# Optimization experiments

Measured on AMD Instinct MI355X. Metric: run time of the kernel, lower is better.

Reference implementation:

```python
import jax, jax.numpy as jnp
import numpy as np

N, F_IN = 4096, 128
UNITS0, HEADS0 = 16, 4   # hidden GraphAttention layer
UNITS1, HEADS1 = 1, 1    # final layer (sigmoid, mean over last axis)


def _glorot(key, shape):
    fan_in, fan_out = shape[0], shape[1]
    std = (2.0 / (fan_in + fan_out)) ** 0.5
    return std * jax.random.normal(key, shape, dtype=jnp.float32)


def setup_inputs() -> dict:
    key = jax.random.key(0)
    ks = jax.random.split(key, 8)
    x = jax.random.normal(ks[0], (N, F_IN), dtype=jnp.float32)
    adj = (jax.random.uniform(ks[1], (N, N)) < 0.01).astype(jnp.float32)
    return {
        "x": x,
        "adj": adj,
        "w0": _glorot(ks[2], (F_IN, UNITS0)),
        "aw1_0": _glorot(ks[3], (UNITS0, HEADS0)),
        "aw2_0": _glorot(ks[4], (UNITS0, HEADS0)),
        "w1": _glorot(ks[5], (UNITS0 * HEADS0, UNITS1)),
        "aw1_1": _glorot(ks[6], (UNITS1, HEADS1)),
        "aw2_1": _glorot(ks[7], (UNITS1, HEADS1)),
    }


def _gat_layer(x, adj, w, aw1, aw2, activation, final_layer):
    h = x @ w                                   # [N, units]
    a1 = h @ aw1                                # [N, H]
    a2 = h @ aw2                                # [N, H]
    # relu(a1_i + a2_j) broadcast -> [N, N, H]
    coeffs = jax.nn.relu(a1[:, None, :] + a2[None, :, :])
    # elementwise adjacency mask then softmax over neighbor axis (axis=1),
    # matching tf.nn.softmax(adj * coeffs[:,:,i], axis=1)
    attn = jax.nn.softmax(adj[:, :, None] * coeffs, axis=1)   # [N, N, H]
    # per-head aggregation then concat heads: [N, H*units]
    out = jnp.einsum('ijh,jd->ihd', attn, h).reshape(h.shape[0], -1)
    if final_layer:
        out = out.mean(axis=-1)                 # [N]
    return activation(out)


def reference(x, adj, w0, aw1_0, aw2_0, w1, aw1_1, aw2_1):
    h = _gat_layer(x, adj, w0, aw1_0, aw2_0, jax.nn.relu, False)   # [N, 64]
    out = _gat_layer(h, adj, w1, aw1_1, aw2_1, jax.nn.sigmoid, True)  # [N]
    return out
```

## Files before the change

### kernel.cpp

```cpp
#include <hip/hip_runtime.h>
#include <hip/hip_bf16.h>

#define N 4096
#define FIN 128
#define U0 16
#define H0 4
#define MAXD 128
#define NGEMM (N / 16)
#define NCSR (N / 2)
#define FSTRIDE 32

__global__ void k1_fused(const float* __restrict__ adj, const float* __restrict__ x,
                         const float* __restrict__ w0, const float* __restrict__ aw1,
                         const float* __restrict__ aw2,
                         int* __restrict__ deg, int* __restrict__ cols,
                         float* __restrict__ F, float* __restrict__ a1,
                         float* __restrict__ partS0) {
    const int t = threadIdx.x;
    if (blockIdx.x < NGEMM) {
        const int bid = blockIdx.x;
        __shared__ float xs[16][FIN + 1];
        __shared__ float ws[FIN][U0];
        __shared__ float hs[16][U0 + 1];
        const int r0 = bid * 16;

        for (int k = t; k < FIN * U0; k += 256) ws[k / U0][k % U0] = w0[k];
        for (int k = t; k < 16 * FIN; k += 256)
            xs[k / FIN][k % FIN] = x[(size_t)(r0 + k / FIN) * FIN + (k % FIN)];
        __syncthreads();

        const int r = t / U0, u = t % U0;
        float acc = 0.f;
        #pragma unroll 8
        for (int k = 0; k < FIN; ++k) acc += xs[r][k] * ws[k][u];
        hs[r][u] = acc;
        F[(size_t)(r0 + r) * FSTRIDE + u] = acc;
        __syncthreads();

        if (t < 16 * H0) {
            const int rr = t / H0, hh = t % H0;
            float s1 = 0.f, s2 = 0.f;
            #pragma unroll
            for (int u2 = 0; u2 < U0; ++u2) {
                float hv = hs[rr][u2];
                s1 += hv * aw1[u2 * H0 + hh];
                s2 += hv * aw2[u2 * H0 + hh];
            }
            a1[(r0 + rr) * H0 + hh] = s1;
            F[(size_t)(r0 + rr) * FSTRIDE + 16 + hh] = s2;
        } else if (t >= 128 && t < 144) {
            const int d = t - 128;
            float s = 0.f;
            #pragma unroll
            for (int rr = 0; rr < 16; ++rr) s += hs[rr][d];
            partS0[bid * 16 + d] = s;
        }
    } else {
        const int rb = (blockIdx.x - NGEMM) * 2;
        const int lane = t & 63, wid = t >> 6;

        __shared__ int cls[2][MAXD];
        __shared__ int wsum[4];
        __shared__ int dgs[2];

        const float4* __restrict__ ar0 =
            reinterpret_cast<const float4*>(adj + (size_t)rb * N);
        const float4* __restrict__ ar1 =
            reinterpret_cast<const float4*>(adj + (size_t)(rb + 1) * N);
        float4 v0[4], v1[4];
        #pragma unroll
        for (int p = 0; p < 4; ++p) v0[p] = ar0[t + 256 * p];
        #pragma unroll
        for (int p = 0; p < 4; ++p) v1[p] = ar1[t + 256 * p];

        #pragma unroll
        for (int rr = 0; rr < 2; ++rr) {
            const float4* v = rr ? v1 : v0;
            int c = 0;
            #pragma unroll
            for (int p = 0; p < 4; ++p)
                c += (v[p].x != 0.f) + (v[p].y != 0.f) + (v[p].z != 0.f) + (v[p].w != 0.f);

            int sc = c;
            #pragma unroll
            for (int s = 1; s < 64; s <<= 1) {
                int u = __shfl_up(sc, s);
                if (lane >= s) sc += u;
            }
            if (rr) __syncthreads();
            if (lane == 63) wsum[wid] = sc;
            __syncthreads();
            int base = 0;
            #pragma unroll
            for (int w2 = 0; w2 < 4; ++w2)
                if (w2 < wid) base += wsum[w2];
            const int off = base + sc - c;
            if (t == 255) dgs[rr] = min(base + sc, MAXD);

            int w = off;
            #pragma unroll
            for (int p = 0; p < 4; ++p) {
                const int j0 = (t + 256 * p) * 4;
                if (v[p].x != 0.f && w < MAXD) cls[rr][w++] = j0;
                if (v[p].y != 0.f && w < MAXD) cls[rr][w++] = j0 + 1;
                if (v[p].z != 0.f && w < MAXD) cls[rr][w++] = j0 + 2;
                if (v[p].w != 0.f && w < MAXD) cls[rr][w++] = j0 + 3;
            }
        }
        __syncthreads();
        if (t < dgs[0]) cols[(size_t)rb * MAXD + t] = cls[0][t];
        const int t2 = t - 128;
        if (t2 >= 0 && t2 < dgs[1] && t2 < 128)
            cols[(size_t)(rb + 1) * MAXD + t2] = cls[1][t2];
        if (t >= dgs[1] + 128 && t2 >= 128) {}
        if (t < 128) {
            const int k2 = t + 128;
            if (k2 < dgs[1]) cols[(size_t)(rb + 1) * MAXD + k2] = cls[1][k2];
        }
        if (t == 0) { deg[rb] = dgs[0]; deg[rb + 1] = dgs[1]; }
    }
}

__global__ void attn0(const float* __restrict__ F, const float* __restrict__ a1,
                      const float* __restrict__ partS0,
                      const int* __restrict__ deg, const int* __restrict__ cols,
                      const float* __restrict__ w1, float* __restrict__ hp) {
    const int i = blockIdx.x;
    const int t = threadIdx.x;
    __shared__ int cls[MAXD];
    __shared__ float red[16][17];
    __shared__ float s0s[16];
    __shared__ float ln[4][64];
    __shared__ float ld[4][64];

    const int dg = deg[i];
    if (t < MAXD) cls[t] = (t < dg) ? cols[(size_t)i * MAXD + t] : 0;

    {
        const int d = t & 15, ch = t >> 4;
        float s = 0.f;
        #pragma unroll
        for (int k = ch; k < 256; k += 16) s += partS0[k * 16 + d];
        red[ch][d] = s;
    }
    __syncthreads();
    if (t < 16) {
        float s2 = 0.f;
        #pragma unroll
        for (int k = 0; k < 16; ++k) s2 += red[k][t];
        s0s[t] = s2;
    }
    __syncthreads();

    const int wid = t >> 6, lane = t & 63;
    const int hh = lane >> 4, d = lane & 15;
    const float a1v = a1[i * H0 + hh];

    float accn = 0.f, accd = 0.f;
    for (int c = 0; ; ++c) {
        const int kb = wid + 16 * c;
        if (kb >= dg) break;
        int ja[4];
        float ms[4];
        #pragma unroll
        for (int q = 0; q < 4; ++q) {
            const int k = kb + 4 * q;
            ja[q] = cls[k < MAXD ? k : 0];
            ms[q] = (k < dg) ? 1.f : 0.f;
        }
        float a2v[4], h0v[4];
        #pragma unroll
        for (int q = 0; q < 4; ++q) {
            const float* __restrict__ fj = F + (size_t)ja[q] * FSTRIDE;
            h0v[q] = fj[d];
            a2v[q] = fj[16 + hh];
        }
        #pragma unroll
        for (int q = 0; q < 4; ++q) {
            float cc = a1v + a2v[q];
            cc = cc > 0.f ? cc : 0.f;
            const float e = (__expf(cc) - 1.f) * ms[q];
            accn = fmaf(e, h0v[q], accn);
            accd += e;
        }
    }
    ln[wid][lane] = accn;
    ld[wid][lane] = accd;
    __syncthreads();

    if (t < 64) {
        const float an = ln[0][t] + ln[1][t] + ln[2][t] + ln[3][t];
        const float ad = ld[0][t] + ld[1][t] + ld[2][t] + ld[3][t];
        float o = (an + s0s[t & 15]) / (ad + (float)N);
        o = o > 0.f ? o : 0.f;

        float pv = o * w1[t];
        #pragma unroll
        for (int off = 32; off; off >>= 1) pv += __shfl_down(pv, off);
        if (t == 0) hp[i] = pv;
    }
}

__global__ void attn1(const float* __restrict__ hp,
                      const float* __restrict__ aw11, const float* __restrict__ aw21,
                      const int* __restrict__ deg, const int* __restrict__ cols,
                      float* __restrict__ out) {
    __shared__ float hps[N];
    __shared__ int cls[4][MAXD];
    __shared__ float s1red[4];
    const int t = threadIdx.x;
    const int w = t >> 6, lane = t & 63;
    const int i0 = blockIdx.x * 4;

    float s = 0.f;
    const float4* __restrict__ hp4 = reinterpret_cast<const float4*>(hp);
    #pragma unroll
    for (int k = t; k < N / 4; k += 256) {
        float4 v = hp4[k];
        reinterpret_cast<float4*>(hps)[k] = v;
        s += v.x + v.y + v.z + v.w;
    }
    for (int k = t; k < 4 * MAXD; k += 256)
        cls[k >> 7][k & 127] = cols[(size_t)(i0 + (k >> 7)) * MAXD + (k & 127)];

    #pragma unroll
    for (int o = 32; o; o >>= 1) s += __shfl_down(s, o);
    if (lane == 0) s1red[w] = s;
    __syncthreads();
    const float S1 = s1red[0] + s1red[1] + s1red[2] + s1red[3];

    const int i = i0 + w;
    const float w1v = aw11[0], w2v = aw21[0];
    const float a1v = hps[i] * w1v;
    const int dg = deg[i];

    float accn = 0.f, accd = 0.f;
    for (int k = lane; k < dg; k += 64) {
        const int j = cls[w][k];
        const float hj = hps[j];
        float cc = a1v + hj * w2v;
        cc = cc > 0.f ? cc : 0.f;
        const float e = __expf(cc) - 1.f;
        accn = fmaf(e, hj, accn);
        accd += e;
    }
    #pragma unroll
    for (int o = 32; o; o >>= 1) {
        accn += __shfl_down(accn, o);
        accd += __shfl_down(accd, o);
    }
    if (lane == 0) {
        const float v = (accn + S1) / (accd + (float)N);
        out[i] = 1.f / (1.f + __expf(-v));
    }
}

extern "C" void kernel_launch(void* const* d_in, const int* in_sizes, int n_in,
                              void* d_out, int out_size, void* d_ws, size_t ws_size,
                              hipStream_t stream) {
    const float* x    = (const float*)d_in[0];
    const float* adj  = (const float*)d_in[1];
    const float* w0   = (const float*)d_in[2];
    const float* aw10 = (const float*)d_in[3];
    const float* aw20 = (const float*)d_in[4];
    const float* w1   = (const float*)d_in[5];
    const float* aw11 = (const float*)d_in[6];
    const float* aw21 = (const float*)d_in[7];
    float* out = (float*)d_out;

    char* p = (char*)d_ws;
    auto alloc = [&](size_t bytes) {
        char* r = p;
        p += (bytes + 255) & ~(size_t)255;
        return r;
    };
    float* partS0 = (float*)alloc(NGEMM * 16 * 4);
    float* F      = (float*)alloc((size_t)N * FSTRIDE * 4);
    float* a1     = (float*)alloc((size_t)N * H0 * 4);
    float* hp     = (float*)alloc((size_t)N * 4);
    int*   deg    = (int*)alloc((size_t)N * 4);
    int*   cols   = (int*)alloc((size_t)N * MAXD * 4);

    k1_fused<<<NGEMM + NCSR, 256, 0, stream>>>(adj, x, w0, aw10, aw20,
                                               deg, cols, F, a1, partS0);
    attn0<<<N, 256, 0, stream>>>(F, a1, partS0, deg, cols, w1, hp);
    attn1<<<N / 4, 256, 0, stream>>>(hp, aw11, aw21, deg, cols, out);
}
```

Before: 38.77 us.

## Atomically accumulate column sums and vectorize neighbor gathers in attn0

Column sums of h are now accumulated with atomicAdd into a 16-float buffer, which is zeroed by a memset beforehand. This removes the per-block reduction of 256 partial sums that every attn0 block used to redo. The attn0 gather is also restructured so each lane loads a float4 of h per neighbor and processes two neighbors per iteration, with the partial results combined by wavefront shuffles instead of shared-memory sums. The change adds a memset launch and makes the S0 sum order nondeterministic.

```diff
diff --git a/kernel.cpp b/kernel.cpp
--- a/kernel.cpp
+++ b/kernel.cpp
@@ -15,7 +15,7 @@
                          const float* __restrict__ aw2,
                          int* __restrict__ deg, int* __restrict__ cols,
                          float* __restrict__ F, float* __restrict__ a1,
-                         float* __restrict__ partS0) {
+                         float* __restrict__ S0) {
     const int t = threadIdx.x;
     if (blockIdx.x < NGEMM) {
         const int bid = blockIdx.x;
@@ -53,7 +53,7 @@
             float s = 0.f;
             #pragma unroll
             for (int rr = 0; rr < 16; ++rr) s += hs[rr][d];
-            partS0[bid * 16 + d] = s;
+            atomicAdd(&S0[d], s);
         }
     } else {
         const int rb = (blockIdx.x - NGEMM) * 2;
@@ -112,7 +112,6 @@
         const int t2 = t - 128;
         if (t2 >= 0 && t2 < dgs[1] && t2 < 128)
             cols[(size_t)(rb + 1) * MAXD + t2] = cls[1][t2];
-        if (t >= dgs[1] + 128 && t2 >= 128) {}
         if (t < 128) {
             const int k2 = t + 128;
             if (k2 < dgs[1]) cols[(size_t)(rb + 1) * MAXD + k2] = cls[1][k2];
@@ -122,76 +121,82 @@
 }
 
 __global__ void attn0(const float* __restrict__ F, const float* __restrict__ a1,
-                      const float* __restrict__ partS0,
+                      const float* __restrict__ S0,
                       const int* __restrict__ deg, const int* __restrict__ cols,
                       const float* __restrict__ w1, float* __restrict__ hp) {
     const int i = blockIdx.x;
     const int t = threadIdx.x;
     __shared__ int cls[MAXD];
-    __shared__ float red[16][17];
-    __shared__ float s0s[16];
-    __shared__ float ln[4][64];
-    __shared__ float ld[4][64];
+    __shared__ float4 lnv[4][16];
+    __shared__ float  ldv[4][4];
+    __shared__ float  rowv[4];
 
     const int dg = deg[i];
     if (t < MAXD) cls[t] = (t < dg) ? cols[(size_t)i * MAXD + t] : 0;
-
-    {
-        const int d = t & 15, ch = t >> 4;
-        float s = 0.f;
-        #pragma unroll
-        for (int k = ch; k < 256; k += 16) s += partS0[k * 16 + d];
-        red[ch][d] = s;
-    }
     __syncthreads();
-    if (t < 16) {
-        float s2 = 0.f;
-        #pragma unroll
-        for (int k = 0; k < 16; ++k) s2 += red[k][t];
-        s0s[t] = s2;
-    }
+
+    const int wid = t >> 6, lane = t & 63;
+    const int q = lane >> 4, r = lane & 15;
+    const int hh = r >> 2, dgc = r & 3;
+    const float a1v = a1[i * H0 + hh];
+
+    float4 accn = make_float4(0.f, 0.f, 0.f, 0.f);
+    float accd = 0.f;
+    for (int kb = 4 * wid; kb < dg; kb += 32) {
+        const int kA = kb + q;
+        const int kB = kb + 16 + q;
+        const int jA = cls[kA < MAXD ? kA : 0];
+        const int jB = cls[kB < MAXD ? kB : 0];
+        const float msA = (kA < dg) ? 1.f : 0.f;
+        const float msB = (kB < dg) ? 1.f : 0.f;
+        const float* __restrict__ fA = F + (size_t)jA * FSTRIDE;
+        const float* __restrict__ fB = F + (size_t)jB * FSTRIDE;
+        const float4 hA = *reinterpret_cast<const float4*>(fA + dgc * 4);
+        const float a2A = fA[16 + hh];
+        const float4 hB = *reinterpret_cast<const float4*>(fB + dgc * 4);
+        const float a2B = fB[16 + hh];
+
+        float ccA = a1v + a2A;
+        ccA = ccA > 0.f ? ccA : 0.f;
+        const float eA = (__expf(ccA) - 1.f) * msA;
+        accn.x = fmaf(eA, hA.x, accn.x);
+        accn.y = fmaf(eA, hA.y, accn.y);
+        accn.z = fmaf(eA, hA.z, accn.z);
+        accn.w = fmaf(eA, hA.w, accn.w);
+        accd += eA;
+
+        float ccB = a1v + a2B;
+        ccB = ccB > 0.f ? ccB : 0.f;
+        const float eB = (__expf(ccB) - 1.f) * msB;
+        accn.x = fmaf(eB, hB.x, accn.x);
+        accn.y = fmaf(eB, hB.y, accn.y);
+        accn.z = fmaf(eB, hB.z, accn.z);
+        accn.w = fmaf(eB, hB.w, accn.w);
+        accd += eB;
+    }
+
+    #pragma unroll
+    for (int m = 16; m <= 32; m <<= 1) {
+        accn.x += __shfl_xor(accn.x, m);
+        accn.y += __shfl_xor(accn.y, m);
+        accn.z += __shfl_xor(accn.z, m);
+        accn.w += __shfl_xor(accn.w, m);
+        accd   += __shfl_xor(accd, m);
+    }
+    if (lane < 16) lnv[wid][r] = accn;
+    if (lane < 16 && dgc == 0) ldv[wid][hh] = accd;
     __syncthreads();
 
-    const int wid = t >> 6, lane = t & 63;
-    const int hh = lane >> 4, d = lane & 15;
-    const float a1v = a1[i * H0 + hh];
-
-    float accn = 0.f, accd = 0.f;
-    for (int c = 0; ; ++c) {
-        const int kb = wid + 16 * c;
-        if (kb >= dg) break;
-        int ja[4];
-        float ms[4];
-        #pragma unroll
-        for (int q = 0; q < 4; ++q) {
-            const int k = kb + 4 * q;
-            ja[q] = cls[k < MAXD ? k : 0];
-            ms[q] = (k < dg) ? 1.f : 0.f;
-        }
-        float a2v[4], h0v[4];
-        #pragma unroll
-        for (int q = 0; q < 4; ++q) {
-            const float* __restrict__ fj = F + (size_t)ja[q] * FSTRIDE;
-            h0v[q] = fj[d];
-            a2v[q] = fj[16 + hh];
-        }
-        #pragma unroll
-        for (int q = 0; q < 4; ++q) {
-            float cc = a1v + a2v[q];
-            cc = cc > 0.f ? cc : 0.f;
-            const float e = (__expf(cc) - 1.f) * ms[q];
-            accn = fmaf(e, h0v[q], accn);
-            accd += e;
-        }
-    }
-    ln[wid][lane] = accn;
-    ld[wid][lane] = accd;
-    __syncthreads();
-
     if (t < 64) {
-        const float an = ln[0][t] + ln[1][t] + ln[2][t] + ln[3][t];
-        const float ad = ld[0][t] + ld[1][t] + ld[2][t] + ld[3][t];
-        float o = (an + s0s[t & 15]) / (ad + (float)N);
+        const int hh_o = t >> 4, d_o = t & 15;
+        const int r_o = hh_o * 4 + (d_o >> 2), c_o = d_o & 3;
+        float an = 0.f, ad = 0.f;
+        #pragma unroll
+        for (int w = 0; w < 4; ++w) {
+            an += reinterpret_cast<const float*>(&lnv[w][r_o])[c_o];
+            ad += ldv[w][hh_o];
+        }
+        float o = (an + S0[d_o]) / (ad + (float)N);
         o = o > 0.f ? o : 0.f;
 
         float pv = o * w1[t];
@@ -274,15 +279,16 @@
         p += (bytes + 255) & ~(size_t)255;
         return r;
     };
-    float* partS0 = (float*)alloc(NGEMM * 16 * 4);
-    float* F      = (float*)alloc((size_t)N * FSTRIDE * 4);
-    float* a1     = (float*)alloc((size_t)N * H0 * 4);
-    float* hp     = (float*)alloc((size_t)N * 4);
-    int*   deg    = (int*)alloc((size_t)N * 4);
-    int*   cols   = (int*)alloc((size_t)N * MAXD * 4);
-
+    float* S0   = (float*)alloc(256);
+    float* F    = (float*)alloc((size_t)N * FSTRIDE * 4);
+    float* a1   = (float*)alloc((size_t)N * H0 * 4);
+    float* hp   = (float*)alloc((size_t)N * 4);
+    int*   deg  = (int*)alloc((size_t)N * 4);
+    int*   cols = (int*)alloc((size_t)N * MAXD * 4);
+
+    hipMemsetAsync(S0, 0, 64, stream);
     k1_fused<<<NGEMM + NCSR, 256, 0, stream>>>(adj, x, w0, aw10, aw20,
-                                               deg, cols, F, a1, partS0);
-    attn0<<<N, 256, 0, stream>>>(F, a1, partS0, deg, cols, w1, hp);
+                                               deg, cols, F, a1, S0);
+    attn0<<<N, 256, 0, stream>>>(F, a1, S0, deg, cols, w1, hp);
     attn1<<<N / 4, 256, 0, stream>>>(hp, aw11, aw21, deg, cols, out);
 }
```

After: 36.67 us. 1.06x faster.
